# Kernel optimization log

Hardware: AMD Instinct MI355X
Metric: run time of the kernel (lower is better)

Reference implementation:

```python
import jax, jax.numpy as jnp
import numpy as np

B, S, D, H, E, K = 2, 1024, 512, 2048, 64, 2
EPS = 1e-5


def setup_inputs() -> dict:
    key = jax.random.key(0)
    ks = jax.random.split(key, 5)
    s = 0.02  # small init scale for stability
    return {
        "x": jax.random.normal(ks[0], (B, S, D), dtype=jnp.float32),
        "Wg": jax.random.normal(ks[1], (D, E), dtype=jnp.float32) * s,
        "bg": jnp.zeros((E,), dtype=jnp.float32),
        "W1": jax.random.normal(ks[2], (E, D, H), dtype=jnp.float32) * s,
        "b1": jnp.zeros((E, H), dtype=jnp.float32),
        "W2": jax.random.normal(ks[3], (E, H, D), dtype=jnp.float32) * s,
        "b2": jnp.zeros((E, D), dtype=jnp.float32),
        "gamma": jnp.ones((D,), dtype=jnp.float32),
        "beta": jnp.zeros((D,), dtype=jnp.float32),
    }


def reference(x, Wg, bg, W1, b1, W2, b2, gamma, beta):
    # Gating: softmax over experts, keep top-k weights, zero the rest (scatter)
    probs = jax.nn.softmax(x @ Wg + bg, axis=-1)          # [B,S,E]
    topk_vals, topk_idx = jax.lax.top_k(probs, K)          # [B,S,K]
    sparse_w = jnp.sum(
        jax.nn.one_hot(topk_idx, E, dtype=probs.dtype) * topk_vals[..., None],
        axis=-2,
    )                                                      # [B,S,E]

    # Dense MoE: run every expert FFN on every token (faithful to source)
    h = jax.nn.relu(jnp.einsum('bsd,edh->bseh', x, W1) + b1)   # [B,S,E,H]
    expert_out = jnp.einsum('bseh,ehd->bsed', h, W2) + b2      # [B,S,E,D]

    # Weighted combine + residual
    out = jnp.einsum('bse,bsed->bsd', sparse_w, expert_out) + x

    # LayerNorm (eps=1e-5, elementwise affine)
    mu = out.mean(-1, keepdims=True)
    var = ((out - mu) ** 2).mean(-1, keepdims=True)
    return (out - mu) * jax.lax.rsqrt(var + EPS) * gamma + beta
```

## Files before the change

### kernel.cpp

```cpp
#include <hip/hip_runtime.h>
#include <hip/hip_bf16.h>

#define NTOK 2048
#define DIM 512
#define HID 2048
#define NEXP 64
#define NSLICE 16
#define HSLICE 128
#define TT 64
#define LN_EPS 1e-5f

#define WS_OFF 0
#define HS_OFF 10240
#define SMEM_BYTES 26624

typedef __bf16 bf16x8 __attribute__((ext_vector_type(8)));
typedef __bf16 bf16x4 __attribute__((ext_vector_type(4)));
typedef float f32x4 __attribute__((ext_vector_type(4)));

__global__ void init_kernel(float4* __restrict__ accb, int* __restrict__ counts) {
    int i = blockIdx.x * blockDim.x + threadIdx.x;
    accb[i] = make_float4(0.f, 0.f, 0.f, 0.f);
    if (i < NEXP) counts[i] = 0;
}

__global__ void gate_kernel(const float* __restrict__ x,
                            const float* __restrict__ Wg,
                            const float* __restrict__ bg,
                            int* __restrict__ counts,
                            int* __restrict__ btok,
                            float* __restrict__ bw) {
    const int t = blockIdx.x;
    const int lane = threadIdx.x;
    __shared__ float xs[DIM];
    const float4* xrow = (const float4*)(x + (size_t)t * DIM);
    ((float4*)xs)[lane] = xrow[lane];
    ((float4*)xs)[lane + 64] = xrow[lane + 64];
    __syncthreads();

    float acc = bg[lane];
    #pragma unroll 8
    for (int d = 0; d < DIM; d++) acc += xs[d] * Wg[d * NEXP + lane];

    float m = acc;
    #pragma unroll
    for (int off = 32; off; off >>= 1) m = fmaxf(m, __shfl_xor(m, off));
    float p = __expf(acc - m);
    float ssum = p;
    #pragma unroll
    for (int off = 32; off; off >>= 1) ssum += __shfl_xor(ssum, off);
    float prob = p / ssum;

    float v1 = prob; int i1 = lane;
    #pragma unroll
    for (int off = 32; off; off >>= 1) {
        float ov = __shfl_xor(v1, off);
        int   oi = __shfl_xor(i1, off);
        if (ov > v1 || (ov == v1 && oi < i1)) { v1 = ov; i1 = oi; }
    }
    float v2 = (lane == i1) ? -1e30f : prob; int i2 = lane;
    #pragma unroll
    for (int off = 32; off; off >>= 1) {
        float ov = __shfl_xor(v2, off);
        int   oi = __shfl_xor(i2, off);
        if (ov > v2 || (ov == v2 && oi < i2)) { v2 = ov; i2 = oi; }
    }

    if (lane == 0) {
        int s0 = atomicAdd(&counts[i1], 1);
        btok[i1 * NTOK + s0] = t;  bw[i1 * NTOK + s0] = v1;
        int s1 = atomicAdd(&counts[i2], 1);
        btok[i2 * NTOK + s1] = t;  bw[i2 * NTOK + s1] = v2;
    }
}

__device__ __forceinline__ int ws_off(int col, int kg) {
    return col * 40 + ((kg ^ ((col >> 3) & 3)) << 3);
}

__global__ __launch_bounds__(256, 4) void ffn_kernel(
    const float* __restrict__ x,
    const float* __restrict__ W1, const float* __restrict__ b1,
    const float* __restrict__ W2, const float* __restrict__ b2,
    const int* __restrict__ counts,
    const int* __restrict__ btok, const float* __restrict__ bw,
    float* __restrict__ accb)
{
    __shared__ char smem[SMEM_BYTES];
    __bf16* wsb = (__bf16*)(smem + WS_OFF);

    const int e = blockIdx.x >> 4;
    const int s = blockIdx.x & 15;
    const int n = counts[e];
    if (n <= 0) return;

    const int tid  = threadIdx.x;
    const int lane = tid & 63;
    const int wid  = tid >> 6;
    const int lq   = lane >> 4;
    const int lm   = lane & 15;
    const int c0   = (tid & 31) * 4;
    const int r0   = (tid >> 5) * 4;

    const float* W1s = W1 + (size_t)e * DIM * HID + s * HSLICE;
    const float* W2s = W2 + ((size_t)e * HID + (size_t)s * HSLICE) * DIM;
    const int*   btoke = btok + e * NTOK;
    const float* bwe   = bw   + e * NTOK;

    for (int t0 = 0; t0 < n; t0 += TT) {
        const int tiln = min(TT, n - t0);

        const int tra = wid * 16 + lm;
        const int tok = btoke[t0 + (tra < tiln ? tra : 0)];
        const float* xrow = x + (size_t)tok * DIM;

        f32x4 acc[8];
        #pragma unroll
        for (int i = 0; i < 8; i++) acc[i] = (f32x4)0.0f;

        for (int ks = 0; ks < 16; ks++) {
            float4 wv[4];
            const float* wp = W1s + (size_t)(ks * 32 + r0) * HID + c0;
            #pragma unroll
            for (int u = 0; u < 4; u++) wv[u] = *(const float4*)(wp + (size_t)u * HID);
            float4 a0 = *(const float4*)(xrow + ks * 32 + lq * 8);
            float4 a1 = *(const float4*)(xrow + ks * 32 + lq * 8 + 4);

            __syncthreads();
            #pragma unroll
            for (int j = 0; j < 4; j++) {
                const float* f0 = (const float*)&wv[0];
                const float* f1 = (const float*)&wv[1];
                const float* f2 = (const float*)&wv[2];
                const float* f3 = (const float*)&wv[3];
                bf16x4 pk;
                pk[0] = (__bf16)f0[j]; pk[1] = (__bf16)f1[j];
                pk[2] = (__bf16)f2[j]; pk[3] = (__bf16)f3[j];
                *(bf16x4*)(wsb + ws_off(c0 + j, r0 >> 3) + (r0 & 7)) = pk;
            }
            bf16x8 af;
            {
                const float* f0 = (const float*)&a0;
                const float* f1 = (const float*)&a1;
                #pragma unroll
                for (int j = 0; j < 4; j++) { af[j] = (__bf16)f0[j]; af[4 + j] = (__bf16)f1[j]; }
            }
            __syncthreads();

            #pragma unroll
            for (int nt = 0; nt < 8; nt++) {
                bf16x8 bfv = *(const bf16x8*)(wsb + ws_off(nt * 16 + lm, lq));
                acc[nt] = __builtin_amdgcn_mfma_f32_16x16x32_bf16(af, bfv, acc[nt], 0, 0, 0);
            }
        }

        #pragma unroll
        for (int nt = 0; nt < 8; nt++) {
            int hloc = nt * 16 + lm;
            float b1v = b1[e * HID + s * HSLICE + hloc];
            #pragma unroll
            for (int r = 0; r < 4; r++) {
                int tr = wid * 16 + lq * 4 + r;
                float v = fmaxf(acc[nt][r] + b1v, 0.f);
                *(__bf16*)(smem + HS_OFF + tr * 256 +
                           (((hloc >> 3) ^ (tr & 7)) * 16) + (hloc & 7) * 2) = (__bf16)v;
            }
        }

        for (int dq = 0; dq < 4; dq++) {
            f32x4 yacc[8];
            #pragma unroll
            for (int i = 0; i < 8; i++) yacc[i] = (f32x4)0.0f;

            for (int ks = 0; ks < 4; ks++) {
                float4 wv[4];
                const float* wp = W2s + (size_t)(ks * 32 + r0) * DIM + dq * 128 + c0;
                #pragma unroll
                for (int u = 0; u < 4; u++) wv[u] = *(const float4*)(wp + (size_t)u * DIM);

                const int trb = wid * 16 + lm;
                bf16x8 af = *(const bf16x8*)(smem + HS_OFF + trb * 256 +
                                             (((ks * 4 + lq) ^ (trb & 7)) * 16));

                __syncthreads();
                #pragma unroll
                for (int j = 0; j < 4; j++) {
                    const float* f0 = (const float*)&wv[0];
                    const float* f1 = (const float*)&wv[1];
                    const float* f2 = (const float*)&wv[2];
                    const float* f3 = (const float*)&wv[3];
                    bf16x4 pk;
                    pk[0] = (__bf16)f0[j]; pk[1] = (__bf16)f1[j];
                    pk[2] = (__bf16)f2[j]; pk[3] = (__bf16)f3[j];
                    *(bf16x4*)(wsb + ws_off(c0 + j, r0 >> 3) + (r0 & 7)) = pk;
                }
                __syncthreads();

                #pragma unroll
                for (int nt = 0; nt < 8; nt++) {
                    bf16x8 bfv = *(const bf16x8*)(wsb + ws_off(nt * 16 + lm, lq));
                    yacc[nt] = __builtin_amdgcn_mfma_f32_16x16x32_bf16(af, bfv, yacc[nt], 0, 0, 0);
                }
            }

            float b2s[8];
            #pragma unroll
            for (int nt = 0; nt < 8; nt++) {
                int d = dq * 128 + nt * 16 + lm;
                b2s[nt] = (s == 0) ? b2[e * DIM + d] : 0.f;
            }
            #pragma unroll
            for (int r = 0; r < 4; r++) {
                int tr = wid * 16 + lq * 4 + r;
                if (tr < tiln) {
                    int tok2 = btoke[t0 + tr];
                    float w = bwe[t0 + tr];
                    float* dst = accb + (size_t)tok2 * DIM;
                    #pragma unroll
                    for (int nt = 0; nt < 8; nt++) {
                        int d = dq * 128 + nt * 16 + lm;
                        atomicAdd(dst + d, w * (yacc[nt][r] + b2s[nt]));
                    }
                }
            }
        }
        __syncthreads();
    }
}

__global__ void ln_kernel(const float* __restrict__ x,
                          const float* __restrict__ accb,
                          const float* __restrict__ gamma,
                          const float* __restrict__ beta,
                          float* __restrict__ out) {
    const int t = blockIdx.x;
    const int tid = threadIdx.x;
    __shared__ float red[8];
    const size_t base = (size_t)t * DIM;
    float v0 = x[base + tid] + accb[base + tid];
    float v1 = x[base + 256 + tid] + accb[base + 256 + tid];
    float s  = v0 + v1;
    float sq = v0 * v0 + v1 * v1;
    #pragma unroll
    for (int off = 32; off; off >>= 1) { s += __shfl_xor(s, off); sq += __shfl_xor(sq, off); }
    if ((tid & 63) == 0) { red[tid >> 6] = s; red[4 + (tid >> 6)] = sq; }
    __syncthreads();
    float S  = red[0] + red[1] + red[2] + red[3];
    float SQ = red[4] + red[5] + red[6] + red[7];
    float mu  = S * (1.f / DIM);
    float var = SQ * (1.f / DIM) - mu * mu;
    float inv = rsqrtf(var + LN_EPS);
    out[base + tid]       = (v0 - mu) * inv * gamma[tid]       + beta[tid];
    out[base + 256 + tid] = (v1 - mu) * inv * gamma[256 + tid] + beta[256 + tid];
}

extern "C" void kernel_launch(void* const* d_in, const int* in_sizes, int n_in,
                              void* d_out, int out_size, void* d_ws, size_t ws_size,
                              hipStream_t stream) {
    const float* x     = (const float*)d_in[0];
    const float* Wg    = (const float*)d_in[1];
    const float* bg    = (const float*)d_in[2];
    const float* W1    = (const float*)d_in[3];
    const float* b1    = (const float*)d_in[4];
    const float* W2    = (const float*)d_in[5];
    const float* b2    = (const float*)d_in[6];
    const float* gamma = (const float*)d_in[7];
    const float* beta  = (const float*)d_in[8];

    char* ws = (char*)d_ws;
    int*   counts = (int*)ws;
    int*   btok   = (int*)(ws + 4096);
    float* bwv    = (float*)(ws + 4096 + 524288);
    float* accb   = (float*)(ws + 4096 + 2 * 524288);

    init_kernel<<<1024, 256, 0, stream>>>((float4*)accb, counts);
    gate_kernel<<<NTOK, 64, 0, stream>>>(x, Wg, bg, counts, btok, bwv);
    ffn_kernel<<<NEXP * NSLICE, 256, 0, stream>>>(x, W1, b1, W2, b2,
                                                  counts, btok, bwv, accb);
    ln_kernel<<<NTOK, 256, 0, stream>>>(x, accb, gamma, beta, (float*)d_out);
}
```

Measured before the change: 684.0 us.

## Process up to 128 tokens per tile to reuse staged expert weights

The token tile per block grows from 64 to 128, processed as two 64-row halves that share each staged bf16 weight chunk in shared memory. Each weight load and fp32-to-bf16 conversion is amortized over twice the MFMA work, reducing weight traffic for experts with more than 64 routed tokens. In exchange the block uses more shared memory and more accumulator registers, and launch bounds drop from 4 to 3 blocks per CU, which lowers occupancy.

```diff
diff --git a/kernel.cpp b/kernel.cpp
--- a/kernel.cpp
+++ b/kernel.cpp
@@ -7,12 +7,12 @@
 #define NEXP 64
 #define NSLICE 16
 #define HSLICE 128
-#define TT 64
+#define TTM 128
 #define LN_EPS 1e-5f
 
 #define WS_OFF 0
 #define HS_OFF 10240
-#define SMEM_BYTES 26624
+#define SMEM_BYTES 43008
 
 typedef __bf16 bf16x8 __attribute__((ext_vector_type(8)));
 typedef __bf16 bf16x4 __attribute__((ext_vector_type(4)));
@@ -78,7 +78,7 @@
     return col * 40 + ((kg ^ ((col >> 3) & 3)) << 3);
 }
 
-__global__ __launch_bounds__(256, 4) void ffn_kernel(
+__global__ __launch_bounds__(256, 3) void ffn_kernel(
     const float* __restrict__ x,
     const float* __restrict__ W1, const float* __restrict__ b1,
     const float* __restrict__ W2, const float* __restrict__ b2,
@@ -107,24 +107,33 @@
     const int*   btoke = btok + e * NTOK;
     const float* bwe   = bw   + e * NTOK;
 
-    for (int t0 = 0; t0 < n; t0 += TT) {
-        const int tiln = min(TT, n - t0);
-
-        const int tra = wid * 16 + lm;
-        const int tok = btoke[t0 + (tra < tiln ? tra : 0)];
-        const float* xrow = x + (size_t)tok * DIM;
-
-        f32x4 acc[8];
+    for (int t0 = 0; t0 < n; t0 += TTM) {
+        const int tiln = min(TTM, n - t0);
+        const bool two = (tiln > 64);
+
+        const int tra0 = wid * 16 + lm;
+        const int tok0 = btoke[t0 + (tra0 < tiln ? tra0 : 0)];
+        const int tra1 = 64 + tra0;
+        const int tok1 = two ? btoke[t0 + (tra1 < tiln ? tra1 : 0)] : tok0;
+        const float* xrow0 = x + (size_t)tok0 * DIM;
+        const float* xrow1 = x + (size_t)tok1 * DIM;
+
+        f32x4 acc0[8], acc1[8];
         #pragma unroll
-        for (int i = 0; i < 8; i++) acc[i] = (f32x4)0.0f;
+        for (int i = 0; i < 8; i++) { acc0[i] = (f32x4)0.0f; acc1[i] = (f32x4)0.0f; }
 
         for (int ks = 0; ks < 16; ks++) {
             float4 wv[4];
             const float* wp = W1s + (size_t)(ks * 32 + r0) * HID + c0;
             #pragma unroll
             for (int u = 0; u < 4; u++) wv[u] = *(const float4*)(wp + (size_t)u * HID);
-            float4 a0 = *(const float4*)(xrow + ks * 32 + lq * 8);
-            float4 a1 = *(const float4*)(xrow + ks * 32 + lq * 8 + 4);
+            float4 a00 = *(const float4*)(xrow0 + ks * 32 + lq * 8);
+            float4 a01 = *(const float4*)(xrow0 + ks * 32 + lq * 8 + 4);
+            float4 a10, a11;
+            if (two) {
+                a10 = *(const float4*)(xrow1 + ks * 32 + lq * 8);
+                a11 = *(const float4*)(xrow1 + ks * 32 + lq * 8 + 4);
+            }
 
             __syncthreads();
             #pragma unroll
@@ -138,19 +147,27 @@
                 pk[2] = (__bf16)f2[j]; pk[3] = (__bf16)f3[j];
                 *(bf16x4*)(wsb + ws_off(c0 + j, r0 >> 3) + (r0 & 7)) = pk;
             }
-            bf16x8 af;
+            bf16x8 af0, af1;
             {
-                const float* f0 = (const float*)&a0;
-                const float* f1 = (const float*)&a1;
-                #pragma unroll
-                for (int j = 0; j < 4; j++) { af[j] = (__bf16)f0[j]; af[4 + j] = (__bf16)f1[j]; }
+                const float* f0 = (const float*)&a00;
+                const float* f1 = (const float*)&a01;
+                #pragma unroll
+                for (int j = 0; j < 4; j++) { af0[j] = (__bf16)f0[j]; af0[4 + j] = (__bf16)f1[j]; }
+            }
+            if (two) {
+                const float* f0 = (const float*)&a10;
+                const float* f1 = (const float*)&a11;
+                #pragma unroll
+                for (int j = 0; j < 4; j++) { af1[j] = (__bf16)f0[j]; af1[4 + j] = (__bf16)f1[j]; }
             }
             __syncthreads();
 
             #pragma unroll
             for (int nt = 0; nt < 8; nt++) {
                 bf16x8 bfv = *(const bf16x8*)(wsb + ws_off(nt * 16 + lm, lq));
-                acc[nt] = __builtin_amdgcn_mfma_f32_16x16x32_bf16(af, bfv, acc[nt], 0, 0, 0);
+                acc0[nt] = __builtin_amdgcn_mfma_f32_16x16x32_bf16(af0, bfv, acc0[nt], 0, 0, 0);
+                if (two)
+                    acc1[nt] = __builtin_amdgcn_mfma_f32_16x16x32_bf16(af1, bfv, acc1[nt], 0, 0, 0);
             }
         }
 
@@ -161,16 +178,22 @@
             #pragma unroll
             for (int r = 0; r < 4; r++) {
                 int tr = wid * 16 + lq * 4 + r;
-                float v = fmaxf(acc[nt][r] + b1v, 0.f);
+                float v = fmaxf(acc0[nt][r] + b1v, 0.f);
                 *(__bf16*)(smem + HS_OFF + tr * 256 +
                            (((hloc >> 3) ^ (tr & 7)) * 16) + (hloc & 7) * 2) = (__bf16)v;
+                if (two) {
+                    int tr1 = 64 + tr;
+                    float v1 = fmaxf(acc1[nt][r] + b1v, 0.f);
+                    *(__bf16*)(smem + HS_OFF + tr1 * 256 +
+                               (((hloc >> 3) ^ (tr1 & 7)) * 16) + (hloc & 7) * 2) = (__bf16)v1;
+                }
             }
         }
 
         for (int dq = 0; dq < 4; dq++) {
-            f32x4 yacc[8];
-            #pragma unroll
-            for (int i = 0; i < 8; i++) yacc[i] = (f32x4)0.0f;
+            f32x4 yacc0[8], yacc1[8];
+            #pragma unroll
+            for (int i = 0; i < 8; i++) { yacc0[i] = (f32x4)0.0f; yacc1[i] = (f32x4)0.0f; }
 
             for (int ks = 0; ks < 4; ks++) {
                 float4 wv[4];
@@ -178,9 +201,15 @@
                 #pragma unroll
                 for (int u = 0; u < 4; u++) wv[u] = *(const float4*)(wp + (size_t)u * DIM);
 
-                const int trb = wid * 16 + lm;
-                bf16x8 af = *(const bf16x8*)(smem + HS_OFF + trb * 256 +
-                                             (((ks * 4 + lq) ^ (trb & 7)) * 16));
+                const int trb0 = wid * 16 + lm;
+                bf16x8 af0 = *(const bf16x8*)(smem + HS_OFF + trb0 * 256 +
+                                              (((ks * 4 + lq) ^ (trb0 & 7)) * 16));
+                bf16x8 af1;
+                if (two) {
+                    const int trb1 = 64 + trb0;
+                    af1 = *(const bf16x8*)(smem + HS_OFF + trb1 * 256 +
+                                           (((ks * 4 + lq) ^ (trb1 & 7)) * 16));
+                }
 
                 __syncthreads();
                 #pragma unroll
@@ -199,7 +228,9 @@
                 #pragma unroll
                 for (int nt = 0; nt < 8; nt++) {
                     bf16x8 bfv = *(const bf16x8*)(wsb + ws_off(nt * 16 + lm, lq));
-                    yacc[nt] = __builtin_amdgcn_mfma_f32_16x16x32_bf16(af, bfv, yacc[nt], 0, 0, 0);
+                    yacc0[nt] = __builtin_amdgcn_mfma_f32_16x16x32_bf16(af0, bfv, yacc0[nt], 0, 0, 0);
+                    if (two)
+                        yacc1[nt] = __builtin_amdgcn_mfma_f32_16x16x32_bf16(af1, bfv, yacc1[nt], 0, 0, 0);
                 }
             }
 
@@ -219,7 +250,20 @@
                     #pragma unroll
                     for (int nt = 0; nt < 8; nt++) {
                         int d = dq * 128 + nt * 16 + lm;
-                        atomicAdd(dst + d, w * (yacc[nt][r] + b2s[nt]));
+                        atomicAdd(dst + d, w * (yacc0[nt][r] + b2s[nt]));
+                    }
+                }
+                if (two) {
+                    int tr1 = 64 + tr;
+                    if (tr1 < tiln) {
+                        int tok2 = btoke[t0 + tr1];
+                        float w = bwe[t0 + tr1];
+                        float* dst = accb + (size_t)tok2 * DIM;
+                        #pragma unroll
+                        for (int nt = 0; nt < 8; nt++) {
+                            int d = dq * 128 + nt * 16 + lm;
+                            atomicAdd(dst + d, w * (yacc1[nt][r] + b2s[nt]));
+                        }
                     }
                 }
             }
```

Result: faster. 651.9 us (-4.7%).
